# Optimization experiments

Measured on AMD Instinct MI355X. Metric: run time of the kernel, lower is better.

Reference implementation:

```python
import jax, jax.numpy as jnp
import numpy as np

B = 131072
COUNT = 8
L1, L2, L3 = 512, 16, 32


def setup_inputs() -> dict:
    key = jax.random.key(0)
    ks = jax.random.split(key, 10)
    return {
        "accum": jax.random.normal(ks[0], (B, 2 * (L1 + COUNT)), dtype=jnp.float32),
        "us": jax.random.uniform(ks[1], (B,), dtype=jnp.float32),
        "l1_w": jax.random.normal(ks[2], (L2 * COUNT, 2 * L1), dtype=jnp.float32) * 0.02,
        "l1_b": jax.random.normal(ks[3], (L2 * COUNT,), dtype=jnp.float32) * 0.02,
        "l2_w": jax.random.normal(ks[4], (L3 * COUNT, L2), dtype=jnp.float32) * 0.05,
        "l2_b": jax.random.normal(ks[5], (L3 * COUNT,), dtype=jnp.float32) * 0.05,
        "out_w": jax.random.normal(ks[6], (COUNT, L3), dtype=jnp.float32) * 0.05,
        "out_b": jax.random.normal(ks[7], (COUNT,), dtype=jnp.float32) * 0.05,
        "psqt_indices": jax.random.randint(ks[8], (B,), 0, COUNT),
        "layer_stack_indices": jax.random.randint(ks[9], (B,), 0, COUNT),
    }


def reference(accum, us, l1_w, l1_b, l2_w, l2_b, out_w, out_b,
              psqt_indices, layer_stack_indices):
    n = accum.shape[0]
    rows = jnp.arange(n)
    lsi = layer_stack_indices.astype(jnp.int32)

    # split accumulator: [w_main(512), w_psqt(8), b_main(512), b_psqt(8)]
    w_main = accum[:, :L1]
    w_psqt = accum[:, L1:L1 + COUNT]
    b_main = accum[:, L1 + COUNT:2 * L1 + COUNT]
    b_psqt = accum[:, 2 * L1 + COUNT:]
    main_accum = jnp.concatenate([w_main, b_main], axis=1)  # [B, 1024]

    # LayerStacks: dense compute over all stacks, then per-sample gather
    l1s = (main_accum @ l1_w.T + l1_b).reshape(n, COUNT, L2)
    l1y = jnp.clip(l1s[rows, lsi], 0.0, 1.0)                # [B, L2]
    l2s = (l1y @ l2_w.T + l2_b).reshape(n, COUNT, L3)
    l2y = jnp.clip(l2s[rows, lsi], 0.0, 1.0)                # [B, L3]
    l3s = (l2y @ out_w.T + out_b)                           # [B, COUNT]
    net_out = l3s[rows, lsi][:, None]                       # [B, 1]

    # psqt combine
    pi = psqt_indices.astype(jnp.int32)[:, None]
    wpsqt = jnp.take_along_axis(w_psqt, pi, axis=1)
    bpsqt = jnp.take_along_axis(b_psqt, pi, axis=1)
    us_ = us.reshape(-1, 1)
    return net_out + (wpsqt - bpsqt) * (us_ - 0.5)
```

## Files before the change

### kernel.cpp

```cpp
#include <hip/hip_runtime.h>
#include <hip/hip_bf16.h>

#define NCOUNT 8
#define B_TOTAL 131072
#define W_WIN 1024
#define BLK 256
#define AT_STRIDE 1048

typedef __attribute__((ext_vector_type(8))) short bf16x8;
typedef __attribute__((ext_vector_type(4))) float f32x4;
typedef __attribute__((ext_vector_type(16))) float f32x16;

__device__ inline short bf_cvt(float x) {
    __hip_bfloat16 h = __float2bfloat16(x);
    return *reinterpret_cast<short*>(&h);
}
__device__ inline bf16x8 cvt8(float4 a, float4 b) {
    bf16x8 r;
    r[0] = bf_cvt(a.x); r[1] = bf_cvt(a.y); r[2] = bf_cvt(a.z); r[3] = bf_cvt(a.w);
    r[4] = bf_cvt(b.x); r[5] = bf_cvt(b.y); r[6] = bf_cvt(b.z); r[7] = bf_cvt(b.w);
    return r;
}

__global__ __launch_bounds__(BLK, 3) void nnue_mfma_kernel(
    const float* __restrict__ accum,
    const float* __restrict__ us,
    const float* __restrict__ l1_w,
    const float* __restrict__ l1_b,
    const float* __restrict__ l2_w,
    const float* __restrict__ l2_b,
    const float* __restrict__ out_w,
    const float* __restrict__ out_b,
    const int*   __restrict__ psqt_indices,
    const int*   __restrict__ lsi,
    float*       __restrict__ out)
{
    __shared__ int list[W_WIN];
    __shared__ int cnt;
    __shared__ __align__(16) short At[16][AT_STRIDE];
    __shared__ __align__(16) float psq[16][16];
    __shared__ __align__(16) float l1part[4][64][4];
    __shared__ __align__(16) float l1y[16 * 20];

    const int l    = blockIdx.y;
    const int base = blockIdx.x * W_WIN;
    const int tid  = threadIdx.x;
    const int lane = tid & 63;
    const int wid  = tid >> 6;

    if (tid == 0) cnt = 0;
    __syncthreads();
    for (int i = tid; i < W_WIN; i += BLK)
        if (lsi[base + i] == l) list[atomicAdd(&cnt, 1)] = base + i;
    __syncthreads();
    const int n = cnt;
    if (n == 0) return;

    const int jlow  = lane & 15;
    const int g     = lane >> 4;
    const int col32 = lane & 31;
    const int h     = lane >> 5;

    const float* wrow = l1_w + (((size_t)l * 16 + jlow) << 10);
    bf16x8 wfrag[8];
    #pragma unroll
    for (int i = 0; i < 8; ++i) {
        const int kf = (wid * 8 + i) * 32 + g * 8;
        wfrag[i] = cvt8(*(const float4*)(wrow + kf), *(const float4*)(wrow + kf + 4));
    }
    const float* w2row = l2_w + ((size_t)l * 32 + col32) * 16 + h * 8;
    const bf16x8 w2frag = cvt8(*(const float4*)(w2row), *(const float4*)(w2row + 4));
    float w3v[16], b2v[16];
    #pragma unroll
    for (int r = 0; r < 16; ++r) {
        int j2 = (r & 3) + 8 * (r >> 2) + 4 * h;
        w3v[r] = out_w[l * 32 + j2];
        b2v[r] = l2_b[l * 32 + j2];
    }
    const float l1bias = l1_b[l * 16 + jlow];
    const float outb   = out_b[l];

    const int srow  = tid >> 5;
    const int scol8 = tid & 31;

    for (int tb = 0; tb < n; tb += 16) {
        #pragma unroll
        for (int rr = 0; rr < 2; ++rr) {
            const int row = rr * 8 + srow;
            const int mi  = tb + row;
            const float* src = accum + (size_t)list[mi < n ? mi : n - 1] * 1040;
            #pragma unroll
            for (int p = 0; p < 4; ++p) {
                const int col = scol8 + 32 * p;
                const int sf  = 8 * col + (col >= 64 ? 8 : 0);
                float4 a0 = *(const float4*)(src + sf);
                float4 a1 = *(const float4*)(src + sf + 4);
                *(bf16x8*)&At[row][8 * col] = cvt8(a0, a1);
            }
        }
        if (tid < 64) {
            const int pr = tid >> 2, part = tid & 3;
            const int mi = tb + pr;
            const float* src = accum + (size_t)list[mi < n ? mi : n - 1] * 1040;
            const int sf = (part < 2) ? (512 + 4 * part) : (1032 + 4 * (part - 2));
            *(float4*)&psq[pr][part * 4] = *(const float4*)(src + sf);
        }
        __syncthreads();

        f32x4 acc = {0.f, 0.f, 0.f, 0.f};
        #pragma unroll
        for (int i = 0; i < 8; ++i) {
            const int kf = (wid * 8 + i) * 32 + g * 8;
            bf16x8 afrag = *(const bf16x8*)&At[jlow][kf];
            acc = __builtin_amdgcn_mfma_f32_16x16x32_bf16(afrag, wfrag[i], acc, 0, 0, 0);
        }
        *(f32x4*)&l1part[wid][lane][0] = acc;
        __syncthreads();

        if (wid == 0) {
            f32x4 t0 = *(const f32x4*)&l1part[0][lane][0];
            f32x4 t1 = *(const f32x4*)&l1part[1][lane][0];
            f32x4 t2 = *(const f32x4*)&l1part[2][lane][0];
            f32x4 t3 = *(const f32x4*)&l1part[3][lane][0];
            #pragma unroll
            for (int r = 0; r < 4; ++r) {
                float v = fminf(fmaxf(t0[r] + t1[r] + t2[r] + t3[r] + l1bias, 0.f), 1.f);
                l1y[(g * 4 + r) * 20 + jlow] = v;
            }
            __builtin_amdgcn_wave_barrier();
            asm volatile("s_waitcnt lgkmcnt(0)" ::: "memory");

            const float* lyr = l1y + (col32 & 15) * 20 + h * 8;
            float4 y0 = *(const float4*)(lyr);
            float4 y1 = *(const float4*)(lyr + 4);
            const bf16x8 b2frag = cvt8(y0, y1);

            f32x16 acc2 = {};
            acc2 = __builtin_amdgcn_mfma_f32_32x32x16_bf16(w2frag, b2frag, acc2, 0, 0, 0);

            float partial = 0.f;
            #pragma unroll
            for (int r = 0; r < 16; ++r) {
                float v = fminf(fmaxf(acc2[r] + b2v[r], 0.f), 1.f);
                partial += v * w3v[r];
            }
            partial += __shfl_xor(partial, 32);

            if (lane < 16 && tb + jlow < n) {
                const int s  = list[tb + jlow];
                const int pi = psqt_indices[s];
                const float wp = psq[jlow][pi];
                const float bp = psq[jlow][8 + pi];
                out[s] = partial + outb + (wp - bp) * (us[s] - 0.5f);
            }
        }
        __syncthreads();
    }
}

extern "C" void kernel_launch(void* const* d_in, const int* in_sizes, int n_in,
                              void* d_out, int out_size, void* d_ws, size_t ws_size,
                              hipStream_t stream) {
    const float* accum = (const float*)d_in[0];
    const float* us    = (const float*)d_in[1];
    const float* l1_w  = (const float*)d_in[2];
    const float* l1_b  = (const float*)d_in[3];
    const float* l2_w  = (const float*)d_in[4];
    const float* l2_b  = (const float*)d_in[5];
    const float* out_w = (const float*)d_in[6];
    const float* out_b = (const float*)d_in[7];
    const int*   psqt  = (const int*)d_in[8];
    const int*   lsi   = (const int*)d_in[9];
    float* out = (float*)d_out;

    dim3 grid(B_TOTAL / W_WIN, NCOUNT);
    nnue_mfma_kernel<<<grid, BLK, 0, stream>>>(
        accum, us, l1_w, l1_b, l2_w, l2_b, out_w, out_b, psqt, lsi, out);
}
```

Measured before the change: 124.3 us.

## Software-prefetch next tile's accumulator rows into registers during MFMA compute

Global loads for the next 16-row tile (main accumulator, psqt slice, us and psqt index) are issued into registers right after the barrier, so their latency overlaps the current tile's MFMA and layer-2 work. The psqt shared buffer is double-buffered so the next tile's write cannot clobber values the current tile still reads. The extra prefetch registers (16 float4 per thread) push launch bounds from 3 to 2 blocks per SM, giving up occupancy-based latency hiding in exchange for explicit overlap.

After: 111.0 us. 10.7% less time.

```diff
diff --git a/kernel.cpp b/kernel.cpp
--- a/kernel.cpp
+++ b/kernel.cpp
@@ -22,7 +22,7 @@
     return r;
 }
 
-__global__ __launch_bounds__(BLK, 3) void nnue_mfma_kernel(
+__global__ __launch_bounds__(BLK, 2) void nnue_mfma_kernel(
     const float* __restrict__ accum,
     const float* __restrict__ us,
     const float* __restrict__ l1_w,
@@ -38,7 +38,7 @@
     __shared__ int list[W_WIN];
     __shared__ int cnt;
     __shared__ __align__(16) short At[16][AT_STRIDE];
-    __shared__ __align__(16) float psq[16][16];
+    __shared__ __align__(16) float psq[2][16][16];
     __shared__ __align__(16) float l1part[4][64][4];
     __shared__ __align__(16) float l1y[16 * 20];
 
@@ -82,30 +82,56 @@
 
     const int srow  = tid >> 5;
     const int scol8 = tid & 31;
-
-    for (int tb = 0; tb < n; tb += 16) {
+    const int pr    = tid >> 2;
+    const int ppart = tid & 3;
+    const int psf   = (ppart < 2) ? (512 + 4 * ppart) : (1032 + 4 * (ppart - 2));
+
+    float4 pfa[8], pfb[8];
+    float4 pfq;
+    float  us_nxt = 0.f; int pi_nxt = 0;
+    float  us_cur;       int pi_cur;
+
+    auto issue_pf = [&](int tb) {
+        #pragma unroll
+        for (int rr = 0; rr < 2; ++rr) {
+            const int mi = tb + rr * 8 + srow;
+            const float* src = accum + (size_t)list[mi < n ? mi : n - 1] * 1040;
+            #pragma unroll
+            for (int p = 0; p < 4; ++p) {
+                const int sf = 8 * (scol8 + 32 * p) + (p >= 2 ? 8 : 0);
+                pfa[rr * 4 + p] = *(const float4*)(src + sf);
+                pfb[rr * 4 + p] = *(const float4*)(src + sf + 4);
+            }
+        }
+        if (tid < 64) {
+            const int mi = tb + pr;
+            const float* src = accum + (size_t)list[mi < n ? mi : n - 1] * 1040;
+            pfq = *(const float4*)(src + psf);
+        }
+        if (wid == 0 && lane < 16) {
+            const int mi = tb + jlow;
+            const int s  = list[mi < n ? mi : n - 1];
+            us_nxt = us[s];
+            pi_nxt = psqt_indices[s];
+        }
+    };
+
+    issue_pf(0);
+
+    int buf = 0;
+    for (int tb = 0; tb < n; tb += 16, buf ^= 1) {
         #pragma unroll
         for (int rr = 0; rr < 2; ++rr) {
             const int row = rr * 8 + srow;
-            const int mi  = tb + row;
-            const float* src = accum + (size_t)list[mi < n ? mi : n - 1] * 1040;
-            #pragma unroll
-            for (int p = 0; p < 4; ++p) {
-                const int col = scol8 + 32 * p;
-                const int sf  = 8 * col + (col >= 64 ? 8 : 0);
-                float4 a0 = *(const float4*)(src + sf);
-                float4 a1 = *(const float4*)(src + sf + 4);
-                *(bf16x8*)&At[row][8 * col] = cvt8(a0, a1);
-            }
-        }
-        if (tid < 64) {
-            const int pr = tid >> 2, part = tid & 3;
-            const int mi = tb + pr;
-            const float* src = accum + (size_t)list[mi < n ? mi : n - 1] * 1040;
-            const int sf = (part < 2) ? (512 + 4 * part) : (1032 + 4 * (part - 2));
-            *(float4*)&psq[pr][part * 4] = *(const float4*)(src + sf);
-        }
+            #pragma unroll
+            for (int p = 0; p < 4; ++p)
+                *(bf16x8*)&At[row][8 * (scol8 + 32 * p)] = cvt8(pfa[rr * 4 + p], pfb[rr * 4 + p]);
+        }
+        if (tid < 64) *(float4*)&psq[buf][pr][ppart * 4] = pfq;
         __syncthreads();
+
+        us_cur = us_nxt; pi_cur = pi_nxt;
+        issue_pf(tb + 16);
 
         f32x4 acc = {0.f, 0.f, 0.f, 0.f};
         #pragma unroll
@@ -147,11 +173,10 @@
             partial += __shfl_xor(partial, 32);
 
             if (lane < 16 && tb + jlow < n) {
-                const int s  = list[tb + jlow];
-                const int pi = psqt_indices[s];
-                const float wp = psq[jlow][pi];
-                const float bp = psq[jlow][8 + pi];
-                out[s] = partial + outb + (wp - bp) * (us[s] - 0.5f);
+                const int s = list[tb + jlow];
+                const float wp = psq[buf][jlow][pi_cur];
+                const float bp = psq[buf][jlow][8 + pi_cur];
+                out[s] = partial + outb + (wp - bp) * (us_cur - 0.5f);
             }
         }
         __syncthreads();
```
